# Optimization experiments

Hardware: AMD Instinct MI355X
Metric: run time of the kernel (lower is better)

The kernel has to match this reference:

```python
import jax, jax.numpy as jnp
import numpy as np

N_GENOMES = 30000
N_GENES = 240000
N_SAMPLES = 128
N_SEQS = 80000


def setup_inputs() -> dict:
    key = jax.random.key(0)
    k0, k1, k2, k3, k4 = jax.random.split(key, 5)
    A = jax.random.normal(k0, (N_GENOMES, N_SAMPLES), dtype=jnp.float32)  # log-abundance
    B = jax.random.normal(k1, (N_GENOMES, N_SAMPLES), dtype=jnp.float32)  # log-PTR
    pos = jax.random.uniform(k2, (N_GENES,), dtype=jnp.float32)           # dist from ori, in [0,1)
    genome_idx = jnp.sort(jax.random.randint(k3, (N_GENES,), 0, N_GENOMES))  # block one-hot of `members`
    seq_idx = jax.random.randint(k4, (N_GENES,), 0, N_SEQS)               # gene -> md5 sequence map
    return {"A": A, "B": B, "pos": pos, "genome_idx": genome_idx, "seq_idx": seq_idx}


def reference(A, B, pos, genome_idx, seq_idx):
    # G = members @ A + 1 - dists @ B, where members/dists are one-hot per gene row
    # -> gather rows of A and B by genome assignment, scale B row by gene position.
    G = A[genome_idx] + 1.0 - pos[:, None] * B[genome_idx]   # (m, s)
    # gene_to_seq @ exp(G) -> segment sum of exp(G) over gene->sequence assignment
    return jax.ops.segment_sum(jnp.exp(G), seq_idx, num_segments=N_SEQS)  # (k, s)
```

## Files before the change

### kernel.cpp

```cpp
#include <hip/hip_runtime.h>
#include <hip/hip_fp16.h>

#define N_GENOMES 30000
#define N_GENES   240000
#define N_SAMPLES 128
#define N_SEQS    80000
#define CAP       32

#define SCATTER_BLOCKS  ((N_GENES + 255) / 256)
#define COMPRESS_BLOCKS ((N_GENOMES * 32) / 256)

typedef float        f32x4 __attribute__((ext_vector_type(4)));
typedef unsigned int u32x4 __attribute__((ext_vector_type(4)));

#define LOG2E 1.4426950408889634f

#if __has_builtin(__builtin_amdgcn_exp2f)
#define EXP2F(x) __builtin_amdgcn_exp2f(x)
#else
#define EXP2F(x) exp2f(x)
#endif

__global__ __launch_bounds__(256) void prep_kernel(
    const float* __restrict__ A,
    const float* __restrict__ B,
    const float* __restrict__ pos,
    const int*   __restrict__ genome_idx,
    const int*   __restrict__ seq_idx,
    int*          __restrict__ cnt,
    unsigned int* __restrict__ bucket0,
    unsigned int* __restrict__ bucketOv,
    float4*       __restrict__ AB16)
{
    int b = blockIdx.x;
    if (b < SCATTER_BLOCKS) {
        int gene = b * 256 + threadIdx.x;
        if (gene >= N_GENES) return;
        int   s = seq_idx[gene];
        int   g = genome_idx[gene];
        float p = pos[gene];
        unsigned int q   = (unsigned int)(p * 131072.0f);
        unsigned int rec = (unsigned int)g | (q << 15);
        int slot = atomicAdd(&cnt[s], 1);
        if (slot < 4)        bucket0[s * 4 + slot] = rec;
        else if (slot < CAP) bucketOv[s * 28 + (slot - 4)] = rec;
    } else {
        int idx = (b - SCATTER_BLOCKS) * 256 + threadIdx.x;
        f32x4 a  = __builtin_nontemporal_load((const f32x4*)A + idx);
        f32x4 bb = __builtin_nontemporal_load((const f32x4*)B + idx);
        __half2 h[4];
        h[0] = __floats2half2_rn((a.x + 1.0f) * LOG2E, (a.y + 1.0f) * LOG2E);
        h[1] = __floats2half2_rn((a.z + 1.0f) * LOG2E, (a.w + 1.0f) * LOG2E);
        h[2] = __floats2half2_rn(bb.x * LOG2E, bb.y * LOG2E);
        h[3] = __floats2half2_rn(bb.z * LOG2E, bb.w * LOG2E);
        int genome = idx >> 5;
        int quad   = idx & 31;
        int qg = quad >> 2, qw = quad & 3;
        AB16[((size_t)qg * N_GENOMES + genome) * 4 + qw] =
            *reinterpret_cast<float4*>(h);
    }
}

__global__ __launch_bounds__(256) void accum_kernel(
    const float4*       __restrict__ AB16,
    const int*          __restrict__ cnt,
    const unsigned int* __restrict__ bucket0,
    const unsigned int* __restrict__ bucketOv,
    float*              __restrict__ out)
{
    int b   = blockIdx.x;
    int qg  = b & 7;
    int tid = threadIdx.x;
    int seq = (b >> 3) * 64 + (tid >> 2);
    int qw  = tid & 3;

    u32x4 r4 = reinterpret_cast<const u32x4*>(bucket0)[seq];
    int   n  = cnt[seq];
    if (n > CAP) n = CAP;

    const float4* T = AB16 + (size_t)qg * N_GENOMES * 4 + qw;

    float4 acc = make_float4(0.f, 0.f, 0.f, 0.f);

    {
        unsigned int r[4] = { r4.x, r4.y, r4.z, r4.w };
        float4 raw[4];
        #pragma unroll
        for (int j = 0; j < 4; ++j) {
            unsigned int g = (j < n) ? (r[j] & 0x7fffu) : 0u;
            raw[j] = T[(size_t)g * 4];
        }
        #pragma unroll
        for (int j = 0; j < 4; ++j) {
            float p = (float)(r[j] >> 15) * (1.0f / 131072.0f);
            const __half2* hp = reinterpret_cast<const __half2*>(&raw[j]);
            float2 a01 = __half22float2(hp[0]);
            float2 a23 = __half22float2(hp[1]);
            float2 b01 = __half22float2(hp[2]);
            float2 b23 = __half22float2(hp[3]);
            if (j < n) {
                acc.x += EXP2F(a01.x - p * b01.x);
                acc.y += EXP2F(a01.y - p * b01.y);
                acc.z += EXP2F(a23.x - p * b23.x);
                acc.w += EXP2F(a23.y - p * b23.y);
            }
        }
    }

    if (n > 4) {
        const u32x4* bkv =
            reinterpret_cast<const u32x4*>(bucketOv + (size_t)seq * 28);
        for (int i0 = 4; i0 < n; i0 += 4) {
            u32x4 t4 = bkv[(i0 - 4) >> 2];
            unsigned int r[4] = { t4.x, t4.y, t4.z, t4.w };
            float4 raw[4];
            #pragma unroll
            for (int j = 0; j < 4; ++j) {
                unsigned int g = (i0 + j < n) ? (r[j] & 0x7fffu) : 0u;
                raw[j] = T[(size_t)g * 4];
            }
            #pragma unroll
            for (int j = 0; j < 4; ++j) {
                float p = (float)(r[j] >> 15) * (1.0f / 131072.0f);
                const __half2* hp = reinterpret_cast<const __half2*>(&raw[j]);
                float2 a01 = __half22float2(hp[0]);
                float2 a23 = __half22float2(hp[1]);
                float2 b01 = __half22float2(hp[2]);
                float2 b23 = __half22float2(hp[3]);
                if (i0 + j < n) {
                    acc.x += EXP2F(a01.x - p * b01.x);
                    acc.y += EXP2F(a01.y - p * b01.y);
                    acc.z += EXP2F(a23.x - p * b23.x);
                    acc.w += EXP2F(a23.y - p * b23.y);
                }
            }
        }
    }

    int quad = (qg << 2) + qw;
    f32x4 o = { acc.x, acc.y, acc.z, acc.w };
    __builtin_nontemporal_store(o, (f32x4*)out + (size_t)seq * 32 + quad);
}

extern "C" void kernel_launch(void* const* d_in, const int* in_sizes, int n_in,
                              void* d_out, int out_size, void* d_ws, size_t ws_size,
                              hipStream_t stream) {
    const float* A    = (const float*)d_in[0];
    const float* B    = (const float*)d_in[1];
    const float* pos  = (const float*)d_in[2];
    const int*   gidx = (const int*)d_in[3];
    const int*   sidx = (const int*)d_in[4];
    float*       out  = (float*)d_out;

    char*         ws       = (char*)d_ws;
    float4*       AB16     = (float4*)ws;
    int*          cnt      = (int*)(ws + (size_t)N_GENOMES * 32 * 16);
    unsigned int* bucket0  = (unsigned int*)(cnt + N_SEQS);
    unsigned int* bucketOv = bucket0 + (size_t)N_SEQS * 4;

    hipMemsetAsync(cnt, 0, N_SEQS * sizeof(int), stream);

    prep_kernel<<<SCATTER_BLOCKS + COMPRESS_BLOCKS, 256, 0, stream>>>(
        A, B, pos, gidx, sidx, cnt, bucket0, bucketOv, AB16);

    accum_kernel<<<(N_SEQS / 64) * 8, 256, 0, stream>>>(
        AB16, cnt, bucket0, bucketOv, out);
}
```

Before: 122.5 us.

## Fuse memset, prep and accumulate into one cooperative persistent kernel

```diff
diff --git a/kernel.cpp b/kernel.cpp
--- a/kernel.cpp
+++ b/kernel.cpp
@@ -1,14 +1,14 @@
 #include <hip/hip_runtime.h>
 #include <hip/hip_fp16.h>
+#include <hip/hip_cooperative_groups.h>
+
+namespace cg = cooperative_groups;
 
 #define N_GENOMES 30000
 #define N_GENES   240000
 #define N_SAMPLES 128
 #define N_SEQS    80000
 #define CAP       32
-
-#define SCATTER_BLOCKS  ((N_GENES + 255) / 256)
-#define COMPRESS_BLOCKS ((N_GENOMES * 32) / 256)
 
 typedef float        f32x4 __attribute__((ext_vector_type(4)));
 typedef unsigned int u32x4 __attribute__((ext_vector_type(4)));
@@ -21,7 +21,7 @@
 #define EXP2F(x) exp2f(x)
 #endif
 
-__global__ __launch_bounds__(256) void prep_kernel(
+__global__ __launch_bounds__(256, 4) void fused_kernel(
     const float* __restrict__ A,
     const float* __restrict__ B,
     const float* __restrict__ pos,
@@ -30,12 +30,23 @@
     int*          __restrict__ cnt,
     unsigned int* __restrict__ bucket0,
     unsigned int* __restrict__ bucketOv,
-    float4*       __restrict__ AB16)
+    float4*       __restrict__ AB16,
+    float*        __restrict__ out)
 {
-    int b = blockIdx.x;
-    if (b < SCATTER_BLOCKS) {
-        int gene = b * 256 + threadIdx.x;
-        if (gene >= N_GENES) return;
+    cg::grid_group grid = cg::this_grid();
+
+    const int b    = blockIdx.x;
+    const int tid  = threadIdx.x;
+    const int gtid = b * 256 + tid;
+    const int GS   = gridDim.x << 8;
+    const int qg   = b & 7;
+    const int bg   = b >> 3;
+    const int bgCount = gridDim.x >> 3;
+
+    for (int i = gtid; i < N_SEQS; i += GS) cnt[i] = 0;
+    grid.sync();
+
+    for (int gene = gtid; gene < N_GENES; gene += GS) {
         int   s = seq_idx[gene];
         int   g = genome_idx[gene];
         float p = pos[gene];
@@ -44,102 +55,103 @@
         int slot = atomicAdd(&cnt[s], 1);
         if (slot < 4)        bucket0[s * 4 + slot] = rec;
         else if (slot < CAP) bucketOv[s * 28 + (slot - 4)] = rec;
-    } else {
-        int idx = (b - SCATTER_BLOCKS) * 256 + threadIdx.x;
-        f32x4 a  = __builtin_nontemporal_load((const f32x4*)A + idx);
-        f32x4 bb = __builtin_nontemporal_load((const f32x4*)B + idx);
-        __half2 h[4];
-        h[0] = __floats2half2_rn((a.x + 1.0f) * LOG2E, (a.y + 1.0f) * LOG2E);
-        h[1] = __floats2half2_rn((a.z + 1.0f) * LOG2E, (a.w + 1.0f) * LOG2E);
-        h[2] = __floats2half2_rn(bb.x * LOG2E, bb.y * LOG2E);
-        h[3] = __floats2half2_rn(bb.z * LOG2E, bb.w * LOG2E);
-        int genome = idx >> 5;
-        int quad   = idx & 31;
-        int qg = quad >> 2, qw = quad & 3;
-        AB16[((size_t)qg * N_GENOMES + genome) * 4 + qw] =
-            *reinterpret_cast<float4*>(h);
     }
-}
-
-__global__ __launch_bounds__(256) void accum_kernel(
-    const float4*       __restrict__ AB16,
-    const int*          __restrict__ cnt,
-    const unsigned int* __restrict__ bucket0,
-    const unsigned int* __restrict__ bucketOv,
-    float*              __restrict__ out)
-{
-    int b   = blockIdx.x;
-    int qg  = b & 7;
-    int tid = threadIdx.x;
-    int seq = (b >> 3) * 64 + (tid >> 2);
-    int qw  = tid & 3;
-
-    u32x4 r4 = reinterpret_cast<const u32x4*>(bucket0)[seq];
-    int   n  = cnt[seq];
-    if (n > CAP) n = CAP;
-
-    const float4* T = AB16 + (size_t)qg * N_GENOMES * 4 + qw;
-
-    float4 acc = make_float4(0.f, 0.f, 0.f, 0.f);
 
     {
-        unsigned int r[4] = { r4.x, r4.y, r4.z, r4.w };
-        float4 raw[4];
-        #pragma unroll
-        for (int j = 0; j < 4; ++j) {
-            unsigned int g = (j < n) ? (r[j] & 0x7fffu) : 0u;
-            raw[j] = T[(size_t)g * 4];
-        }
-        #pragma unroll
-        for (int j = 0; j < 4; ++j) {
-            float p = (float)(r[j] >> 15) * (1.0f / 131072.0f);
-            const __half2* hp = reinterpret_cast<const __half2*>(&raw[j]);
-            float2 a01 = __half22float2(hp[0]);
-            float2 a23 = __half22float2(hp[1]);
-            float2 b01 = __half22float2(hp[2]);
-            float2 b23 = __half22float2(hp[3]);
-            if (j < n) {
-                acc.x += EXP2F(a01.x - p * b01.x);
-                acc.y += EXP2F(a01.y - p * b01.y);
-                acc.z += EXP2F(a23.x - p * b23.x);
-                acc.w += EXP2F(a23.y - p * b23.y);
+        const int sliceThreads = bgCount << 8;
+        for (int genome = bg * 256 + tid; genome < N_GENOMES; genome += sliceThreads) {
+            const f32x4* Ar = (const f32x4*)(A + (size_t)genome * 128 + qg * 16);
+            const f32x4* Br = (const f32x4*)(B + (size_t)genome * 128 + qg * 16);
+            float4* dst = AB16 + ((size_t)qg * N_GENOMES + genome) * 4;
+            #pragma unroll
+            for (int qw = 0; qw < 4; ++qw) {
+                f32x4 a  = __builtin_nontemporal_load(Ar + qw);
+                f32x4 bb = __builtin_nontemporal_load(Br + qw);
+                __half2 h[4];
+                h[0] = __floats2half2_rn((a.x + 1.0f) * LOG2E, (a.y + 1.0f) * LOG2E);
+                h[1] = __floats2half2_rn((a.z + 1.0f) * LOG2E, (a.w + 1.0f) * LOG2E);
+                h[2] = __floats2half2_rn(bb.x * LOG2E, bb.y * LOG2E);
+                h[3] = __floats2half2_rn(bb.z * LOG2E, bb.w * LOG2E);
+                dst[qw] = *reinterpret_cast<float4*>(h);
             }
         }
     }
 
-    if (n > 4) {
-        const u32x4* bkv =
-            reinterpret_cast<const u32x4*>(bucketOv + (size_t)seq * 28);
-        for (int i0 = 4; i0 < n; i0 += 4) {
-            u32x4 t4 = bkv[(i0 - 4) >> 2];
-            unsigned int r[4] = { t4.x, t4.y, t4.z, t4.w };
-            float4 raw[4];
-            #pragma unroll
-            for (int j = 0; j < 4; ++j) {
-                unsigned int g = (i0 + j < n) ? (r[j] & 0x7fffu) : 0u;
-                raw[j] = T[(size_t)g * 4];
-            }
-            #pragma unroll
-            for (int j = 0; j < 4; ++j) {
-                float p = (float)(r[j] >> 15) * (1.0f / 131072.0f);
-                const __half2* hp = reinterpret_cast<const __half2*>(&raw[j]);
-                float2 a01 = __half22float2(hp[0]);
-                float2 a23 = __half22float2(hp[1]);
-                float2 b01 = __half22float2(hp[2]);
-                float2 b23 = __half22float2(hp[3]);
-                if (i0 + j < n) {
-                    acc.x += EXP2F(a01.x - p * b01.x);
-                    acc.y += EXP2F(a01.y - p * b01.y);
-                    acc.z += EXP2F(a23.x - p * b23.x);
-                    acc.w += EXP2F(a23.y - p * b23.y);
+    grid.sync();
+
+    {
+        const int per  = (N_SEQS + bgCount - 1) / bgCount;
+        const int seq0 = bg * per;
+        const int send = (seq0 + per < N_SEQS) ? seq0 + per : N_SEQS;
+        const int qw   = tid & 3;
+        const float4* T = AB16 + (size_t)qg * N_GENOMES * 4 + qw;
+
+        for (int seq = seq0 + (tid >> 2); seq < send; seq += 64) {
+            u32x4 r4 = reinterpret_cast<const u32x4*>(bucket0)[seq];
+            int   n  = cnt[seq];
+            if (n > CAP) n = CAP;
+
+            float4 acc = make_float4(0.f, 0.f, 0.f, 0.f);
+
+            {
+                unsigned int r[4] = { r4.x, r4.y, r4.z, r4.w };
+                float4 raw[4];
+                #pragma unroll
+                for (int j = 0; j < 4; ++j) {
+                    unsigned int g = (j < n) ? (r[j] & 0x7fffu) : 0u;
+                    raw[j] = T[(size_t)g * 4];
+                }
+                #pragma unroll
+                for (int j = 0; j < 4; ++j) {
+                    float p = (float)(r[j] >> 15) * (1.0f / 131072.0f);
+                    const __half2* hp = reinterpret_cast<const __half2*>(&raw[j]);
+                    float2 a01 = __half22float2(hp[0]);
+                    float2 a23 = __half22float2(hp[1]);
+                    float2 b01 = __half22float2(hp[2]);
+                    float2 b23 = __half22float2(hp[3]);
+                    if (j < n) {
+                        acc.x += EXP2F(a01.x - p * b01.x);
+                        acc.y += EXP2F(a01.y - p * b01.y);
+                        acc.z += EXP2F(a23.x - p * b23.x);
+                        acc.w += EXP2F(a23.y - p * b23.y);
+                    }
                 }
             }
+
+            if (n > 4) {
+                const u32x4* bkv =
+                    reinterpret_cast<const u32x4*>(bucketOv + (size_t)seq * 28);
+                for (int i0 = 4; i0 < n; i0 += 4) {
+                    u32x4 t4 = bkv[(i0 - 4) >> 2];
+                    unsigned int r[4] = { t4.x, t4.y, t4.z, t4.w };
+                    float4 raw[4];
+                    #pragma unroll
+                    for (int j = 0; j < 4; ++j) {
+                        unsigned int g = (i0 + j < n) ? (r[j] & 0x7fffu) : 0u;
+                        raw[j] = T[(size_t)g * 4];
+                    }
+                    #pragma unroll
+                    for (int j = 0; j < 4; ++j) {
+                        float p = (float)(r[j] >> 15) * (1.0f / 131072.0f);
+                        const __half2* hp = reinterpret_cast<const __half2*>(&raw[j]);
+                        float2 a01 = __half22float2(hp[0]);
+                        float2 a23 = __half22float2(hp[1]);
+                        float2 b01 = __half22float2(hp[2]);
+                        float2 b23 = __half22float2(hp[3]);
+                        if (i0 + j < n) {
+                            acc.x += EXP2F(a01.x - p * b01.x);
+                            acc.y += EXP2F(a01.y - p * b01.y);
+                            acc.z += EXP2F(a23.x - p * b23.x);
+                            acc.w += EXP2F(a23.y - p * b23.y);
+                        }
+                    }
+                }
+            }
+
+            f32x4 o = { acc.x, acc.y, acc.z, acc.w };
+            __builtin_nontemporal_store(o, (f32x4*)out + (size_t)seq * 32 + (qg << 2) + qw);
         }
     }
-
-    int quad = (qg << 2) + qw;
-    f32x4 o = { acc.x, acc.y, acc.z, acc.w };
-    __builtin_nontemporal_store(o, (f32x4*)out + (size_t)seq * 32 + quad);
 }
 
 extern "C" void kernel_launch(void* const* d_in, const int* in_sizes, int n_in,
@@ -158,11 +170,17 @@
     unsigned int* bucket0  = (unsigned int*)(cnt + N_SEQS);
     unsigned int* bucketOv = bucket0 + (size_t)N_SEQS * 4;
 
-    hipMemsetAsync(cnt, 0, N_SEQS * sizeof(int), stream);
+    int blocksPerCU = 0;
+    (void)hipOccupancyMaxActiveBlocksPerMultiprocessor(
+        &blocksPerCU, (const void*)fused_kernel, 256, 0);
+    int nblk = blocksPerCU * 256;
+    if (nblk > 1024) nblk = 1024;
+    nblk &= ~7;
+    if (nblk < 8) nblk = 8;
 
-    prep_kernel<<<SCATTER_BLOCKS + COMPRESS_BLOCKS, 256, 0, stream>>>(
-        A, B, pos, gidx, sidx, cnt, bucket0, bucketOv, AB16);
-
-    accum_kernel<<<(N_SEQS / 64) * 8, 256, 0, stream>>>(
-        AB16, cnt, bucket0, bucketOv, out);
+    void* args[] = { (void*)&A, (void*)&B, (void*)&pos, (void*)&gidx, (void*)&sidx,
+                     (void*)&cnt, (void*)&bucket0, (void*)&bucketOv,
+                     (void*)&AB16, (void*)&out };
+    (void)hipLaunchCooperativeKernel((const void*)fused_kernel,
+                                     dim3(nblk), dim3(256), args, 0, stream);
 }
```

Measured after the change: 337.3 us. 175% more time.
